# Performance work log

Hardware: AMD Instinct MI355X
Metric: run time of the kernel (lower is better)

The kernel has to match this reference:

```python
import jax, jax.numpy as jnp
import numpy as np
import math

# ---- module hyperparams (from init_kwargs) ----
L = 10            # number of hash-grid levels
DIM = 4           # features per level
LOG2T = 16
T = 1 << LOG2T    # hash table size per level
BASE = 16         # base resolution
PLS = 2.0         # per_level_scale
SCALE_MULTI = 0.5
HID = 64
IN_DIM = L * DIM  # 40
OUT_DIM = 13      # 1 + 12
N = 1_000_000

# growth factor b = exp((ln(finest) - ln(base)) / (L - 1)), finest = base * pls**L
B_GROWTH = math.exp((math.log(BASE * PLS ** L) - math.log(BASE)) / (L - 1))
RES = [int(math.floor(BASE * B_GROWTH ** l)) for l in range(L)]

PRIMES = np.array([1, 2654435761, 805459861], dtype=np.uint32)
# 8 corner offsets of a voxel
OFFS = np.array([[i, j, k] for i in (0, 1) for j in (0, 1) for k in (0, 1)], dtype=np.uint32)


def _hash_coords(c):
    # c: uint32 [N, 8, 3] -> int32 [N, 8] indices into table of size T
    p = jnp.asarray(PRIMES)
    h = (c[..., 0] * p[0]) ^ (c[..., 1] * p[1]) ^ (c[..., 2] * p[2])
    return (h & jnp.uint32(T - 1)).astype(jnp.int32)


def _encode(x, tables):
    # x: [N,3] in [0,1]; tables: [L, T, DIM] -> [N, DIM, L]
    offs_u = jnp.asarray(OFFS)                      # uint32 [8,3]
    offs_b = jnp.asarray(OFFS.astype(bool))         # bool   [8,3]
    feats = []
    for l in range(L):
        xs = x * RES[l]
        bottom = jnp.floor(xs)
        frac = xs - bottom                          # [N,3]
        corners = bottom.astype(jnp.uint32)[:, None, :] + offs_u[None]  # [N,8,3]
        idx = _hash_coords(corners)                 # [N,8]
        cf = tables[l][idx]                         # [N,8,DIM] gather
        # trilinear weights: prod over dims of frac (if offset==1) else (1-frac)
        w = jnp.prod(jnp.where(offs_b[None], frac[:, None, :], 1.0 - frac[:, None, :]), axis=-1)  # [N,8]
        feats.append(jnp.einsum('nc,ncd->nd', w, cf))  # [N,DIM]
    return jnp.stack(feats, axis=-1)                # [N, DIM, L]


def setup_inputs() -> dict:
    key = jax.random.key(0)
    ks = jax.random.split(key, 10)
    x = jax.random.uniform(ks[0], (N, 3), dtype=jnp.float32)
    cr = jax.random.uniform(ks[1], (N,), dtype=jnp.float32)
    tables = jax.random.uniform(ks[2], (L, T, DIM), dtype=jnp.float32, minval=-1e-4, maxval=1e-4)
    gain = math.sqrt(2.0)  # calculate_gain('relu')

    def xavier(k, fan_in, fan_out):
        a = gain * math.sqrt(6.0 / (fan_in + fan_out))
        return jax.random.uniform(k, (fan_in, fan_out), dtype=jnp.float32, minval=-a, maxval=a)

    W1 = xavier(ks[3], IN_DIM, HID)
    b1 = jnp.zeros((HID,), jnp.float32)
    W2 = xavier(ks[4], HID, HID)
    b2 = jnp.zeros((HID,), jnp.float32)
    W3 = xavier(ks[5], HID, OUT_DIM)
    b3 = jnp.zeros((OUT_DIM,), jnp.float32)
    return {"x": x, "cr": cr, "tables": tables,
            "W1": W1, "b1": b1, "W2": W2, "b2": b2, "W3": W3, "b3": b3}


def reference(x, cr, tables, W1, b1, W2, b2, W3, b3):
    enc = _encode(x, tables)                        # [N, DIM, L]
    cr_s = cr.reshape(-1) * SCALE_MULTI             # [N]
    n = jnp.arange(L, dtype=jnp.float32).reshape(1, 1, L)
    denom = PLS * 4.0 * n * cr_s[:, None, None]     # [N,1,L]
    erf_x = 1.0 / jnp.sqrt(jnp.maximum(denom, 1e-12))  # safe_div/safe_sqrt; erf(huge)=1 at n=0
    scaling = jax.lax.erf(erf_x)
    h = (enc * scaling).reshape(-1, IN_DIM)         # [N, 40]
    h = jax.nn.selu(h @ W1 + b1)
    h = jax.nn.selu(h @ W2 + b2)
    return h @ W3 + b3                              # [N, 13]
```

## Files before the change

kernel.cpp:

```cpp
#include <hip/hip_runtime.h>
#include <cmath>

typedef unsigned int uint32;
typedef __bf16 bf16;
typedef __bf16 bf16x8 __attribute__((ext_vector_type(8)));
typedef float f32x4 __attribute__((ext_vector_type(4)));

#define LVLS 10
#define TSIZE 65536
#define TMASK 65535u
#define PRIME2 2654435761u
#define PRIME3 805459861u

#define WOFF_W1 0
#define WOFF_W2 4096
#define WOFF_W3 8192
#define W_ELEMS 9216
#define DQ_OFF 18432
#define SC_OFF 18496
#define TAB_OFF_B 18560
#define TAB_ELEMS_F (LVLS * TSIZE * 4)
#define WS_NEEDED ((size_t)TAB_OFF_B + (size_t)TAB_ELEMS_F)

struct KParams { float resf[LVLS]; };

__global__ void scale_kernel(const float* __restrict__ tables, unsigned* __restrict__ scales) {
  int tid = blockIdx.x * 256 + threadIdx.x;
  int i4 = tid * 4;
  if (i4 >= TAB_ELEMS_F) return;
  float4 v = *(const float4*)(tables + i4);
  float m = fmaxf(fmaxf(fabsf(v.x), fabsf(v.y)), fmaxf(fabsf(v.z), fabsf(v.w)));
#pragma unroll
  for (int off = 32; off; off >>= 1) m = fmaxf(m, __shfl_xor(m, off, 64));
  if ((threadIdx.x & 63) == 0) {
    int l = i4 >> 18;
    atomicMax(scales + l, __float_as_uint(m));
  }
}

__global__ void quant_kernel(const float* __restrict__ W1, const float* __restrict__ W2,
                             const float* __restrict__ W3, const float* __restrict__ tables,
                             char* __restrict__ ws8, int do_tab) {
  int tid = blockIdx.x * 256 + threadIdx.x;
  bf16* wsb = (bf16*)ws8;
  if (tid < W_ELEMS) {
    float v;
    if (tid < 4096) {
      int n = tid >> 6, kp_ = tid & 63;
      if (kp_ < 40) {
        int l = kp_ >> 2, d = kp_ & 3;
        v = W1[(d * 10 + l) * 64 + n];
      } else v = 0.f;
    } else if (tid < 8192) {
      int t2 = tid - 4096; int n = t2 >> 6, k = t2 & 63;
      v = W2[k * 64 + n];
    } else {
      int t3 = tid - 8192; int n = t3 >> 6, k = t3 & 63;
      v = (n < 13) ? W3[k * 13 + n] : 0.f;
    }
    wsb[tid] = (bf16)v;
  }
  const unsigned* scales = (const unsigned*)(ws8 + SC_OFF);
  if (tid < LVLS) {
    float s = __uint_as_float(scales[tid]);
    ((float*)(ws8 + DQ_OFF))[tid] = s * (1.0f / 127.0f);
  }
  if (do_tab) {
    int i4 = tid * 4;
    if (i4 < TAB_ELEMS_F) {
      float4 v = *(const float4*)(tables + i4);
      int l = i4 >> 18;
      float s = __uint_as_float(scales[l]);
      float r = (s > 0.f) ? 127.f / s : 0.f;
      int q0 = (int)rintf(fminf(fmaxf(v.x * r, -127.f), 127.f)) + 128;
      int q1 = (int)rintf(fminf(fmaxf(v.y * r, -127.f), 127.f)) + 128;
      int q2 = (int)rintf(fminf(fmaxf(v.z * r, -127.f), 127.f)) + 128;
      int q3 = (int)rintf(fminf(fmaxf(v.w * r, -127.f), 127.f)) + 128;
      unsigned p = (q0 & 0xff) | ((q1 & 0xff) << 8) | ((q2 & 0xff) << 16) | ((q3 & 0xff) << 24);
      *(unsigned*)(ws8 + TAB_OFF_B + i4) = p;
    }
  }
}

__device__ __forceinline__ float selu_f(float v) {
  float neg = 1.6732632423543772f * (__expf(v) - 1.0f);
  return 1.0507009873554805f * (v > 0.f ? v : neg);
}

__device__ __forceinline__ bf16* hswz(bf16* Hb, int row, int cb) {
  return (bf16*)((char*)Hb + (row << 7) + (cb ^ ((row & 7) << 4)));
}

__device__ __forceinline__ void gemm_stage(bf16* __restrict__ Hb, int w, int lr, int quad,
                                           const bf16* __restrict__ Bbase,
                                           const float* __restrict__ bvec) {
  bf16x8 Af[2][4];
#pragma unroll
  for (int ks = 0; ks < 2; ++ks)
#pragma unroll
    for (int ms = 0; ms < 4; ++ms)
      Af[ks][ms] = *(const bf16x8*)hswz(Hb, w * 64 + ms * 16 + lr, quad * 16 + ks * 64);
#pragma unroll
  for (int h = 0; h < 2; ++h) {
    f32x4 acc[4][2];
#pragma unroll
    for (int nt2 = 0; nt2 < 2; ++nt2) {
      float b = bvec[(h * 2 + nt2) * 16 + lr];
#pragma unroll
      for (int ms = 0; ms < 4; ++ms) {
        f32x4 a = {b, b, b, b};
        acc[ms][nt2] = a;
      }
    }
#pragma unroll
    for (int ks = 0; ks < 2; ++ks) {
      bf16x8 B0 = *(const bf16x8*)(Bbase + (h * 2 + 0) * 1024 + ks * 32);
      bf16x8 B1 = *(const bf16x8*)(Bbase + (h * 2 + 1) * 1024 + ks * 32);
#pragma unroll
      for (int ms = 0; ms < 4; ++ms) {
        acc[ms][0] = __builtin_amdgcn_mfma_f32_16x16x32_bf16(Af[ks][ms], B0, acc[ms][0], 0, 0, 0);
        acc[ms][1] = __builtin_amdgcn_mfma_f32_16x16x32_bf16(Af[ks][ms], B1, acc[ms][1], 0, 0, 0);
      }
    }
#pragma unroll
    for (int ms = 0; ms < 4; ++ms)
#pragma unroll
      for (int nt2 = 0; nt2 < 2; ++nt2)
#pragma unroll
        for (int r = 0; r < 4; ++r) {
          int row = w * 64 + quad * 4 + ms * 16 + r;
          *hswz(Hb, row, ((h * 2 + nt2) * 16 + lr) * 2) = (bf16)selu_f(acc[ms][nt2][r]);
        }
  }
}

#define CALC_IDX(L, IDX, F0, F1, F2)                                   \
  do {                                                                 \
    const float rs_ = kp.resf[(L)];                                    \
    float xs_ = px * rs_, ys_ = py * rs_, zs_ = pz * rs_;              \
    float bx_ = floorf(xs_), by_ = floorf(ys_), bz_ = floorf(zs_);     \
    (F0) = xs_ - bx_; (F1) = ys_ - by_; (F2) = zs_ - bz_;              \
    uint32 cx_ = (uint32)bx_, cy_ = (uint32)by_, cz_ = (uint32)bz_;    \
    uint32 hy0_ = cy_ * PRIME2, hy1_ = hy0_ + PRIME2;                  \
    uint32 hz0_ = cz_ * PRIME3, hz1_ = hz0_ + PRIME3;                  \
    uint32 cx1_ = cx_ + 1u;                                            \
    uint32 bse_ = (uint32)(L) << 16;                                   \
    (IDX)[0] = ((cx_ ^ hy0_ ^ hz0_) & TMASK) | bse_;                   \
    (IDX)[1] = ((cx_ ^ hy0_ ^ hz1_) & TMASK) | bse_;                   \
    (IDX)[2] = ((cx_ ^ hy1_ ^ hz0_) & TMASK) | bse_;                   \
    (IDX)[3] = ((cx_ ^ hy1_ ^ hz1_) & TMASK) | bse_;                   \
    (IDX)[4] = ((cx1_ ^ hy0_ ^ hz0_) & TMASK) | bse_;                  \
    (IDX)[5] = ((cx1_ ^ hy0_ ^ hz1_) & TMASK) | bse_;                  \
    (IDX)[6] = ((cx1_ ^ hy1_ ^ hz0_) & TMASK) | bse_;                  \
    (IDX)[7] = ((cx1_ ^ hy1_ ^ hz1_) & TMASK) | bse_;                  \
  } while (0)

template <bool TB>
__global__ __launch_bounds__(256, 4)
void ngp_fused(const float* __restrict__ x, const float* __restrict__ cr,
               const float* __restrict__ tables, const char* __restrict__ ws8,
               const float* __restrict__ b1, const float* __restrict__ b2,
               const float* __restrict__ b3, float* __restrict__ out,
               int N, KParams kp) {
  __shared__ __align__(16) bf16 Hbuf[256 * 64];
  const int tid = threadIdx.x;
  const int n = blockIdx.x * 256 + tid;
  const int ncl = (n < N) ? n : 0;

  const float px = x[ncl * 3 + 0];
  const float py = x[ncl * 3 + 1];
  const float pz = x[ncl * 3 + 2];
  const float crv = cr[ncl];
  const float* dq = (const float*)(ws8 + DQ_OFF);

#pragma unroll
  for (int g = 0; g < 5; ++g) {
    bf16x8 v;
#pragma unroll
    for (int h = 0; h < 2; ++h) {
      const int l = g * 2 + h;
      uint32 idx[8];
      float fx, fy, fz;
      CALC_IDX(l, idx, fx, fy, fz);
      float a0 = 0.f, a1 = 0.f, a2 = 0.f, a3 = 0.f;
      if constexpr (TB) {
        const unsigned* tb = (const unsigned*)(ws8 + TAB_OFF_B);
        unsigned q[8];
#pragma unroll
        for (int c = 0; c < 8; ++c) q[c] = tb[idx[c]];
        float wx1 = fx, wx0 = 1.f - fx, wy1 = fy, wy0 = 1.f - fy, wz1 = fz, wz0 = 1.f - fz;
        float wxy00 = wx0 * wy0, wxy01 = wx0 * wy1, wxy10 = wx1 * wy0, wxy11 = wx1 * wy1;
        float w8[8] = {wxy00 * wz0, wxy00 * wz1, wxy01 * wz0, wxy01 * wz1,
                       wxy10 * wz0, wxy10 * wz1, wxy11 * wz0, wxy11 * wz1};
#pragma unroll
        for (int c = 0; c < 8; ++c) {
          unsigned q_ = q[c];
          a0 = fmaf(w8[c], (float)(q_ & 0xffu), a0);
          a1 = fmaf(w8[c], (float)((q_ >> 8) & 0xffu), a1);
          a2 = fmaf(w8[c], (float)((q_ >> 16) & 0xffu), a2);
          a3 = fmaf(w8[c], (float)(q_ >> 24), a3);
        }
        float s = (l == 0) ? dq[0]
                           : erff(rsqrtf(fmaxf(4.0f * (float)l * crv, 1e-12f))) * dq[l];
        v[h * 4 + 0] = (bf16)((a0 - 128.f) * s);
        v[h * 4 + 1] = (bf16)((a1 - 128.f) * s);
        v[h * 4 + 2] = (bf16)((a2 - 128.f) * s);
        v[h * 4 + 3] = (bf16)((a3 - 128.f) * s);
      } else {
        const float4* tb4 = (const float4*)tables;
        float f[8][4];
#pragma unroll
        for (int c = 0; c < 8; ++c) {
          float4 q = tb4[idx[c]];
          f[c][0] = q.x; f[c][1] = q.y; f[c][2] = q.z; f[c][3] = q.w;
        }
        float wx1 = fx, wx0 = 1.f - fx, wy1 = fy, wy0 = 1.f - fy, wz1 = fz, wz0 = 1.f - fz;
        float wxy00 = wx0 * wy0, wxy01 = wx0 * wy1, wxy10 = wx1 * wy0, wxy11 = wx1 * wy1;
        float w8[8] = {wxy00 * wz0, wxy00 * wz1, wxy01 * wz0, wxy01 * wz1,
                       wxy10 * wz0, wxy10 * wz1, wxy11 * wz0, wxy11 * wz1};
#pragma unroll
        for (int c = 0; c < 8; ++c) {
          a0 = fmaf(w8[c], f[c][0], a0);
          a1 = fmaf(w8[c], f[c][1], a1);
          a2 = fmaf(w8[c], f[c][2], a2);
          a3 = fmaf(w8[c], f[c][3], a3);
        }
        float s = (l == 0) ? 1.0f : erff(rsqrtf(fmaxf(4.0f * (float)l * crv, 1e-12f)));
        v[h * 4 + 0] = (bf16)(a0 * s);
        v[h * 4 + 1] = (bf16)(a1 * s);
        v[h * 4 + 2] = (bf16)(a2 * s);
        v[h * 4 + 3] = (bf16)(a3 * s);
      }
    }
    *(bf16x8*)hswz(Hbuf, tid, g * 16) = v;
  }
  {
    bf16x8 z;
#pragma unroll
    for (int j = 0; j < 8; ++j) z[j] = (bf16)0.f;
    *(bf16x8*)hswz(Hbuf, tid, 80) = z;
    *(bf16x8*)hswz(Hbuf, tid, 96) = z;
    *(bf16x8*)hswz(Hbuf, tid, 112) = z;
  }
  __syncthreads();

  const int w = tid >> 6;
  const int lane = tid & 63;
  const int lr = lane & 15;
  const int quad = lane >> 4;
  const bf16* wsb = (const bf16*)ws8;

  gemm_stage(Hbuf, w, lr, quad, wsb + WOFF_W1 + lr * 64 + quad * 8, b1);
  __syncthreads();
  gemm_stage(Hbuf, w, lr, quad, wsb + WOFF_W2 + lr * 64 + quad * 8, b2);
  __syncthreads();

  {
    float b3v = (lr < 13) ? b3[lr] : 0.f;
    f32x4 acc3[4];
#pragma unroll
    for (int ms = 0; ms < 4; ++ms) {
      f32x4 a = {b3v, b3v, b3v, b3v};
      acc3[ms] = a;
    }
    const bf16* B3b = wsb + WOFF_W3 + lr * 64 + quad * 8;
    bf16x8 B3[2];
    B3[0] = *(const bf16x8*)(B3b);
    B3[1] = *(const bf16x8*)(B3b + 32);
#pragma unroll
    for (int ks = 0; ks < 2; ++ks) {
      bf16x8 Af[4];
#pragma unroll
      for (int ms = 0; ms < 4; ++ms)
        Af[ms] = *(const bf16x8*)hswz(Hbuf, w * 64 + ms * 16 + lr, quad * 16 + ks * 64);
#pragma unroll
      for (int ms = 0; ms < 4; ++ms)
        acc3[ms] = __builtin_amdgcn_mfma_f32_16x16x32_bf16(Af[ms], B3[ks], acc3[ms], 0, 0, 0);
    }
    __syncthreads();
    float* Obuf = (float*)Hbuf;
#pragma unroll
    for (int ms = 0; ms < 4; ++ms)
#pragma unroll
      for (int r = 0; r < 4; ++r)
        if (lr < 13)
          Obuf[(w * 64 + quad * 4 + ms * 16 + r) * 13 + lr] = acc3[ms][r];
    __syncthreads();

    const int base = blockIdx.x * 256;
    int nrows = N - base;
    if (nrows >= 256) {
      float4* og4 = (float4*)(out + (size_t)base * 13);
      const float4* Ob4 = (const float4*)Obuf;
#pragma unroll
      for (int i = 0; i < 4; ++i) {
        int j = tid + i * 256;
        if (j < 832) og4[j] = Ob4[j];
      }
    } else {
      const int nfl = nrows * 13;
      float* og = out + (size_t)base * 13;
      for (int j = tid; j < nfl; j += 256) og[j] = Obuf[j];
    }
  }
}

extern "C" void kernel_launch(void* const* d_in, const int* in_sizes, int n_in,
                              void* d_out, int out_size, void* d_ws, size_t ws_size,
                              hipStream_t stream) {
  const float* x      = (const float*)d_in[0];
  const float* cr     = (const float*)d_in[1];
  const float* tables = (const float*)d_in[2];
  const float* W1     = (const float*)d_in[3];
  const float* b1     = (const float*)d_in[4];
  const float* W2     = (const float*)d_in[5];
  const float* b2     = (const float*)d_in[6];
  const float* W3     = (const float*)d_in[7];
  const float* b3     = (const float*)d_in[8];
  float* out = (float*)d_out;
  const int N = in_sizes[1];

  KParams kp;
  double B = exp((log(16.0 * pow(2.0, 10.0)) - log(16.0)) / 9.0);
  for (int l = 0; l < LVLS; ++l) kp.resf[l] = (float)floor(16.0 * pow(B, (double)l));

  char* ws8 = (char*)d_ws;
  const bool tb = ws_size >= WS_NEEDED;

  const int qblocks = (TAB_ELEMS_F / 4 + 255) / 256;
  if (tb) {
    hipMemsetAsync(ws8 + SC_OFF, 0, 64, stream);
    scale_kernel<<<qblocks, 256, 0, stream>>>(tables, (unsigned*)(ws8 + SC_OFF));
    quant_kernel<<<qblocks, 256, 0, stream>>>(W1, W2, W3, tables, ws8, 1);
  } else {
    quant_kernel<<<(W_ELEMS + 255) / 256, 256, 0, stream>>>(W1, W2, W3, tables, ws8, 0);
  }

  int blocks = (N + 255) / 256;
  if (tb)
    ngp_fused<true><<<blocks, 256, 0, stream>>>(x, cr, tables, ws8, b1, b2, b3, out, N, kp);
  else
    ngp_fused<false><<<blocks, 256, 0, stream>>>(x, cr, tables, ws8, b1, b2, b3, out, N, kp);
}
```

Before: 478.8 us.

## Split hash-grid levels across two threads per point, halve block rows

Each point is now encoded by two threads, one handling even levels and the other odd levels, so a 256-thread block covers 128 points. The GEMM stages shrink to 32 rows per wave, the shared buffer is halved, and launch bounds are raised to 8 blocks per CU to raise occupancy. W1 packing is reordered to match the new interleaved feature layout. The aim is more memory-level parallelism for the gather-bound encoding. In exchange the x/cr loads are duplicated across thread pairs and there is less MFMA work per sync.

```diff
diff --git a/kernel.cpp b/kernel.cpp
--- a/kernel.cpp
+++ b/kernel.cpp
@@ -4,6 +4,7 @@
 typedef unsigned int uint32;
 typedef __bf16 bf16;
 typedef __bf16 bf16x8 __attribute__((ext_vector_type(8)));
+typedef __bf16 bf16x4 __attribute__((ext_vector_type(4)));
 typedef float f32x4 __attribute__((ext_vector_type(4)));
 
 #define LVLS 10
@@ -48,7 +49,8 @@
     if (tid < 4096) {
       int n = tid >> 6, kp_ = tid & 63;
       if (kp_ < 40) {
-        int l = kp_ >> 2, d = kp_ & 3;
+        int i = kp_ >> 3, h = (kp_ >> 2) & 1, d = kp_ & 3;
+        int l = 2 * i + h;
         v = W1[(d * 10 + l) * 64 + n];
       } else v = 0.f;
     } else if (tid < 8192) {
@@ -94,20 +96,20 @@
 __device__ __forceinline__ void gemm_stage(bf16* __restrict__ Hb, int w, int lr, int quad,
                                            const bf16* __restrict__ Bbase,
                                            const float* __restrict__ bvec) {
-  bf16x8 Af[2][4];
+  bf16x8 Af[2][2];
 #pragma unroll
   for (int ks = 0; ks < 2; ++ks)
 #pragma unroll
-    for (int ms = 0; ms < 4; ++ms)
-      Af[ks][ms] = *(const bf16x8*)hswz(Hb, w * 64 + ms * 16 + lr, quad * 16 + ks * 64);
+    for (int ms = 0; ms < 2; ++ms)
+      Af[ks][ms] = *(const bf16x8*)hswz(Hb, w * 32 + ms * 16 + lr, quad * 16 + ks * 64);
 #pragma unroll
   for (int h = 0; h < 2; ++h) {
-    f32x4 acc[4][2];
+    f32x4 acc[2][2];
 #pragma unroll
     for (int nt2 = 0; nt2 < 2; ++nt2) {
       float b = bvec[(h * 2 + nt2) * 16 + lr];
 #pragma unroll
-      for (int ms = 0; ms < 4; ++ms) {
+      for (int ms = 0; ms < 2; ++ms) {
         f32x4 a = {b, b, b, b};
         acc[ms][nt2] = a;
       }
@@ -117,26 +119,26 @@
       bf16x8 B0 = *(const bf16x8*)(Bbase + (h * 2 + 0) * 1024 + ks * 32);
       bf16x8 B1 = *(const bf16x8*)(Bbase + (h * 2 + 1) * 1024 + ks * 32);
 #pragma unroll
-      for (int ms = 0; ms < 4; ++ms) {
+      for (int ms = 0; ms < 2; ++ms) {
         acc[ms][0] = __builtin_amdgcn_mfma_f32_16x16x32_bf16(Af[ks][ms], B0, acc[ms][0], 0, 0, 0);
         acc[ms][1] = __builtin_amdgcn_mfma_f32_16x16x32_bf16(Af[ks][ms], B1, acc[ms][1], 0, 0, 0);
       }
     }
 #pragma unroll
-    for (int ms = 0; ms < 4; ++ms)
+    for (int ms = 0; ms < 2; ++ms)
 #pragma unroll
       for (int nt2 = 0; nt2 < 2; ++nt2)
 #pragma unroll
         for (int r = 0; r < 4; ++r) {
-          int row = w * 64 + quad * 4 + ms * 16 + r;
+          int row = w * 32 + ms * 16 + quad * 4 + r;
           *hswz(Hb, row, ((h * 2 + nt2) * 16 + lr) * 2) = (bf16)selu_f(acc[ms][nt2][r]);
         }
   }
 }
 
-#define CALC_IDX(L, IDX, F0, F1, F2)                                   \
+#define CALC_IDX(LV, RS, IDX, F0, F1, F2)                              \
   do {                                                                 \
-    const float rs_ = kp.resf[(L)];                                    \
+    const float rs_ = (RS);                                            \
     float xs_ = px * rs_, ys_ = py * rs_, zs_ = pz * rs_;              \
     float bx_ = floorf(xs_), by_ = floorf(ys_), bz_ = floorf(zs_);     \
     (F0) = xs_ - bx_; (F1) = ys_ - by_; (F2) = zs_ - bz_;              \
@@ -144,7 +146,7 @@
     uint32 hy0_ = cy_ * PRIME2, hy1_ = hy0_ + PRIME2;                  \
     uint32 hz0_ = cz_ * PRIME3, hz1_ = hz0_ + PRIME3;                  \
     uint32 cx1_ = cx_ + 1u;                                            \
-    uint32 bse_ = (uint32)(L) << 16;                                   \
+    uint32 bse_ = (uint32)(LV) << 16;                                  \
     (IDX)[0] = ((cx_ ^ hy0_ ^ hz0_) & TMASK) | bse_;                   \
     (IDX)[1] = ((cx_ ^ hy0_ ^ hz1_) & TMASK) | bse_;                   \
     (IDX)[2] = ((cx_ ^ hy1_ ^ hz0_) & TMASK) | bse_;                   \
@@ -156,15 +158,17 @@
   } while (0)
 
 template <bool TB>
-__global__ __launch_bounds__(256, 4)
+__global__ __launch_bounds__(256, 8)
 void ngp_fused(const float* __restrict__ x, const float* __restrict__ cr,
                const float* __restrict__ tables, const char* __restrict__ ws8,
                const float* __restrict__ b1, const float* __restrict__ b2,
                const float* __restrict__ b3, float* __restrict__ out,
                int N, KParams kp) {
-  __shared__ __align__(16) bf16 Hbuf[256 * 64];
+  __shared__ __align__(16) bf16 Hbuf[128 * 64];
   const int tid = threadIdx.x;
-  const int n = blockIdx.x * 256 + tid;
+  const int h = tid & 1;
+  const int prow = tid >> 1;
+  const int n = blockIdx.x * 128 + prow;
   const int ncl = (n < N) ? n : 0;
 
   const float px = x[ncl * 3 + 0];
@@ -174,73 +178,74 @@
   const float* dq = (const float*)(ws8 + DQ_OFF);
 
 #pragma unroll
-  for (int g = 0; g < 5; ++g) {
-    bf16x8 v;
-#pragma unroll
-    for (int h = 0; h < 2; ++h) {
-      const int l = g * 2 + h;
-      uint32 idx[8];
-      float fx, fy, fz;
-      CALC_IDX(l, idx, fx, fy, fz);
-      float a0 = 0.f, a1 = 0.f, a2 = 0.f, a3 = 0.f;
-      if constexpr (TB) {
-        const unsigned* tb = (const unsigned*)(ws8 + TAB_OFF_B);
-        unsigned q[8];
-#pragma unroll
-        for (int c = 0; c < 8; ++c) q[c] = tb[idx[c]];
-        float wx1 = fx, wx0 = 1.f - fx, wy1 = fy, wy0 = 1.f - fy, wz1 = fz, wz0 = 1.f - fz;
-        float wxy00 = wx0 * wy0, wxy01 = wx0 * wy1, wxy10 = wx1 * wy0, wxy11 = wx1 * wy1;
-        float w8[8] = {wxy00 * wz0, wxy00 * wz1, wxy01 * wz0, wxy01 * wz1,
-                       wxy10 * wz0, wxy10 * wz1, wxy11 * wz0, wxy11 * wz1};
-#pragma unroll
-        for (int c = 0; c < 8; ++c) {
-          unsigned q_ = q[c];
-          a0 = fmaf(w8[c], (float)(q_ & 0xffu), a0);
-          a1 = fmaf(w8[c], (float)((q_ >> 8) & 0xffu), a1);
-          a2 = fmaf(w8[c], (float)((q_ >> 16) & 0xffu), a2);
-          a3 = fmaf(w8[c], (float)(q_ >> 24), a3);
-        }
-        float s = (l == 0) ? dq[0]
-                           : erff(rsqrtf(fmaxf(4.0f * (float)l * crv, 1e-12f))) * dq[l];
-        v[h * 4 + 0] = (bf16)((a0 - 128.f) * s);
-        v[h * 4 + 1] = (bf16)((a1 - 128.f) * s);
-        v[h * 4 + 2] = (bf16)((a2 - 128.f) * s);
-        v[h * 4 + 3] = (bf16)((a3 - 128.f) * s);
-      } else {
-        const float4* tb4 = (const float4*)tables;
-        float f[8][4];
-#pragma unroll
-        for (int c = 0; c < 8; ++c) {
-          float4 q = tb4[idx[c]];
-          f[c][0] = q.x; f[c][1] = q.y; f[c][2] = q.z; f[c][3] = q.w;
-        }
-        float wx1 = fx, wx0 = 1.f - fx, wy1 = fy, wy0 = 1.f - fy, wz1 = fz, wz0 = 1.f - fz;
-        float wxy00 = wx0 * wy0, wxy01 = wx0 * wy1, wxy10 = wx1 * wy0, wxy11 = wx1 * wy1;
-        float w8[8] = {wxy00 * wz0, wxy00 * wz1, wxy01 * wz0, wxy01 * wz1,
-                       wxy10 * wz0, wxy10 * wz1, wxy11 * wz0, wxy11 * wz1};
-#pragma unroll
-        for (int c = 0; c < 8; ++c) {
-          a0 = fmaf(w8[c], f[c][0], a0);
-          a1 = fmaf(w8[c], f[c][1], a1);
-          a2 = fmaf(w8[c], f[c][2], a2);
-          a3 = fmaf(w8[c], f[c][3], a3);
-        }
-        float s = (l == 0) ? 1.0f : erff(rsqrtf(fmaxf(4.0f * (float)l * crv, 1e-12f)));
-        v[h * 4 + 0] = (bf16)(a0 * s);
-        v[h * 4 + 1] = (bf16)(a1 * s);
-        v[h * 4 + 2] = (bf16)(a2 * s);
-        v[h * 4 + 3] = (bf16)(a3 * s);
-      }
-    }
-    *(bf16x8*)hswz(Hbuf, tid, g * 16) = v;
+  for (int i = 0; i < 5; ++i) {
+    const int l = 2 * i + h;
+    const float rs = h ? kp.resf[2 * i + 1] : kp.resf[2 * i];
+    uint32 idx[8];
+    float fx, fy, fz;
+    CALC_IDX(l, rs, idx, fx, fy, fz);
+    float a0 = 0.f, a1 = 0.f, a2 = 0.f, a3 = 0.f;
+    bf16x4 v;
+    if constexpr (TB) {
+      const unsigned* tb = (const unsigned*)(ws8 + TAB_OFF_B);
+      unsigned q[8];
+#pragma unroll
+      for (int c = 0; c < 8; ++c) q[c] = tb[idx[c]];
+      float wx1 = fx, wx0 = 1.f - fx, wy1 = fy, wy0 = 1.f - fy, wz1 = fz, wz0 = 1.f - fz;
+      float wxy00 = wx0 * wy0, wxy01 = wx0 * wy1, wxy10 = wx1 * wy0, wxy11 = wx1 * wy1;
+      float w8[8] = {wxy00 * wz0, wxy00 * wz1, wxy01 * wz0, wxy01 * wz1,
+                     wxy10 * wz0, wxy10 * wz1, wxy11 * wz0, wxy11 * wz1};
+#pragma unroll
+      for (int c = 0; c < 8; ++c) {
+        unsigned q_ = q[c];
+        a0 = fmaf(w8[c], (float)(q_ & 0xffu), a0);
+        a1 = fmaf(w8[c], (float)((q_ >> 8) & 0xffu), a1);
+        a2 = fmaf(w8[c], (float)((q_ >> 16) & 0xffu), a2);
+        a3 = fmaf(w8[c], (float)(q_ >> 24), a3);
+      }
+      float dql = h ? dq[2 * i + 1] : dq[2 * i];
+      float s = erff(rsqrtf(fmaxf(4.0f * (float)l * crv, 1e-12f))) * dql;
+      v[0] = (bf16)((a0 - 128.f) * s);
+      v[1] = (bf16)((a1 - 128.f) * s);
+      v[2] = (bf16)((a2 - 128.f) * s);
+      v[3] = (bf16)((a3 - 128.f) * s);
+    } else {
+      const float4* tb4 = (const float4*)tables;
+      float f[8][4];
+#pragma unroll
+      for (int c = 0; c < 8; ++c) {
+        float4 q = tb4[idx[c]];
+        f[c][0] = q.x; f[c][1] = q.y; f[c][2] = q.z; f[c][3] = q.w;
+      }
+      float wx1 = fx, wx0 = 1.f - fx, wy1 = fy, wy0 = 1.f - fy, wz1 = fz, wz0 = 1.f - fz;
+      float wxy00 = wx0 * wy0, wxy01 = wx0 * wy1, wxy10 = wx1 * wy0, wxy11 = wx1 * wy1;
+      float w8[8] = {wxy00 * wz0, wxy00 * wz1, wxy01 * wz0, wxy01 * wz1,
+                     wxy10 * wz0, wxy10 * wz1, wxy11 * wz0, wxy11 * wz1};
+#pragma unroll
+      for (int c = 0; c < 8; ++c) {
+        a0 = fmaf(w8[c], f[c][0], a0);
+        a1 = fmaf(w8[c], f[c][1], a1);
+        a2 = fmaf(w8[c], f[c][2], a2);
+        a3 = fmaf(w8[c], f[c][3], a3);
+      }
+      float s = erff(rsqrtf(fmaxf(4.0f * (float)l * crv, 1e-12f)));
+      v[0] = (bf16)(a0 * s);
+      v[1] = (bf16)(a1 * s);
+      v[2] = (bf16)(a2 * s);
+      v[3] = (bf16)(a3 * s);
+    }
+    *(bf16x4*)hswz(Hbuf, prow, i * 16 + h * 8) = v;
   }
   {
     bf16x8 z;
 #pragma unroll
     for (int j = 0; j < 8; ++j) z[j] = (bf16)0.f;
-    *(bf16x8*)hswz(Hbuf, tid, 80) = z;
-    *(bf16x8*)hswz(Hbuf, tid, 96) = z;
-    *(bf16x8*)hswz(Hbuf, tid, 112) = z;
+    if (h == 0) {
+      *(bf16x8*)hswz(Hbuf, prow, 80) = z;
+      *(bf16x8*)hswz(Hbuf, prow, 112) = z;
+    } else {
+      *(bf16x8*)hswz(Hbuf, prow, 96) = z;
+    }
   }
   __syncthreads();
 
@@ -257,9 +262,9 @@
 
   {
     float b3v = (lr < 13) ? b3[lr] : 0.f;
-    f32x4 acc3[4];
-#pragma unroll
-    for (int ms = 0; ms < 4; ++ms) {
+    f32x4 acc3[2];
+#pragma unroll
+    for (int ms = 0; ms < 2; ++ms) {
       f32x4 a = {b3v, b3v, b3v, b3v};
       acc3[ms] = a;
     }
@@ -269,33 +274,33 @@
     B3[1] = *(const bf16x8*)(B3b + 32);
 #pragma unroll
     for (int ks = 0; ks < 2; ++ks) {
-      bf16x8 Af[4];
-#pragma unroll
-      for (int ms = 0; ms < 4; ++ms)
-        Af[ms] = *(const bf16x8*)hswz(Hbuf, w * 64 + ms * 16 + lr, quad * 16 + ks * 64);
-#pragma unroll
-      for (int ms = 0; ms < 4; ++ms)
+      bf16x8 Af[2];
+#pragma unroll
+      for (int ms = 0; ms < 2; ++ms)
+        Af[ms] = *(const bf16x8*)hswz(Hbuf, w * 32 + ms * 16 + lr, quad * 16 + ks * 64);
+#pragma unroll
+      for (int ms = 0; ms < 2; ++ms)
         acc3[ms] = __builtin_amdgcn_mfma_f32_16x16x32_bf16(Af[ms], B3[ks], acc3[ms], 0, 0, 0);
     }
     __syncthreads();
     float* Obuf = (float*)Hbuf;
 #pragma unroll
-    for (int ms = 0; ms < 4; ++ms)
+    for (int ms = 0; ms < 2; ++ms)
 #pragma unroll
       for (int r = 0; r < 4; ++r)
         if (lr < 13)
-          Obuf[(w * 64 + quad * 4 + ms * 16 + r) * 13 + lr] = acc3[ms][r];
+          Obuf[(w * 32 + ms * 16 + quad * 4 + r) * 13 + lr] = acc3[ms][r];
     __syncthreads();
 
-    const int base = blockIdx.x * 256;
+    const int base = blockIdx.x * 128;
     int nrows = N - base;
-    if (nrows >= 256) {
+    if (nrows >= 128) {
       float4* og4 = (float4*)(out + (size_t)base * 13);
       const float4* Ob4 = (const float4*)Obuf;
 #pragma unroll
-      for (int i = 0; i < 4; ++i) {
+      for (int i = 0; i < 2; ++i) {
         int j = tid + i * 256;
-        if (j < 832) og4[j] = Ob4[j];
+        if (j < 416) og4[j] = Ob4[j];
       }
     } else {
       const int nfl = nrows * 13;
@@ -336,7 +341,7 @@
     quant_kernel<<<(W_ELEMS + 255) / 256, 256, 0, stream>>>(W1, W2, W3, tables, ws8, 0);
   }
 
-  int blocks = (N + 255) / 256;
+  int blocks = (N + 127) / 128;
   if (tb)
     ngp_fused<true><<<blocks, 256, 0, stream>>>(x, cr, tables, ws8, b1, b2, b3, out, N, kp);
   else
```

Result: slower. 585.6 us (+22.3%).
